# Kernel tuning notes

Measured on AMD Instinct MI355X. Metric: run time of the kernel, lower is better.

The kernel has to match this reference:

```python
import jax, jax.numpy as jnp
import numpy as np

N_RES = 500000


def _rot(vals):
    # stack 9 scalars-per-element into (..., 3, 3) row-major rotation matrices
    return jnp.stack(vals, axis=-1).reshape(*vals[0].shape, 3, 3)


def _dihedral(p0, p1, p2, p3):
    b0 = -(p1 - p0)
    b1 = p2 - p1
    b2 = p3 - p2
    b0xb1 = jnp.cross(b0, b1)
    b1xb2 = jnp.cross(b2, b1)
    y = jnp.sum(jnp.cross(b0xb1, b1xb2) * b1, axis=-1) / jnp.linalg.norm(b1, axis=-1)
    x = jnp.sum(b0xb1 * b1xb2, axis=-1)
    return jnp.nan_to_num(jnp.arctan2(y, x))


def _bb_dihedrals(N, CA, C):
    phi_ = _dihedral(C[:-1], N[1:], CA[1:], C[1:])
    psi_ = _dihedral(N[:-1], CA[:-1], C[:-1], N[1:])
    omg_ = _dihedral(CA[:-1], C[:-1], N[1:], CA[1:])
    pad = jnp.zeros_like(phi_[:1])
    omega = jnp.concatenate([omg_, pad])
    phi = jnp.concatenate([pad, phi_])
    psi = jnp.concatenate([psi_, pad])
    return jnp.stack([omega, phi, psi], axis=-1)  # (n, 3)


def _frames_from_reference(n_xyz, ca_xyz, c_xyz, eps=1e-20):
    # OpenFold Rigid.make_transform_from_reference
    n = n_xyz - ca_xyz
    c = c_xyz - ca_xyz
    cx, cy, cz = c[..., 0], c[..., 1], c[..., 2]
    z = jnp.zeros_like(cx)
    o = jnp.ones_like(cx)
    nrm = jnp.sqrt(eps + cx**2 + cy**2)
    s1, c1 = -cy / nrm, cx / nrm
    R1 = _rot([c1, -s1, z, s1, c1, z, z, z, o])
    nrm2 = jnp.sqrt(eps + cx**2 + cy**2 + cz**2)
    s2, c2 = cz / nrm2, jnp.sqrt(cx**2 + cy**2) / nrm2
    R2 = _rot([c2, z, s2, z, o, z, -s2, z, c2])
    Rc = R2 @ R1
    n2 = jnp.einsum('...ij,...j->...i', Rc, n)
    ny, nz_ = n2[..., 1], n2[..., 2]
    nrm3 = jnp.sqrt(eps + ny**2 + nz_**2)
    sn, cn = -nz_ / nrm3, ny / nrm3
    Rn = _rot([o, z, z, z, cn, -sn, z, sn, cn])
    rots = jnp.swapaxes(Rn @ Rc, -1, -2)
    return rots, ca_xyz  # (n,3,3), (n,3)


def _compose(ra, ta, rb, tb):
    # rigid composition: (ra,ta) o (rb,tb)
    return ra @ rb, jnp.einsum('...ij,...j->...i', ra, tb) + ta


def _forward(aa, bb_coords, sc_torsions, default_frames, group_idx, atom_mask, lit_positions):
    n_xyz, ca_xyz, c_xyz = bb_coords[:, 0], bb_coords[:, 1], bb_coords[:, 2]
    bb_r, bb_t = _frames_from_reference(n_xyz, ca_xyz, c_xyz)

    angles = jnp.concatenate([_bb_dihedrals(n_xyz, ca_xyz, c_xyz), sc_torsions], axis=-1)  # (n,7)
    alpha = jnp.stack([jnp.sin(angles), jnp.cos(angles)], axis=-1)  # (n,7,2) [sin, cos]
    bb_pad = jnp.concatenate([
        jnp.zeros((alpha.shape[0], 1, 1), alpha.dtype),
        jnp.ones((alpha.shape[0], 1, 1), alpha.dtype)], axis=-1)
    alpha = jnp.concatenate([bb_pad, alpha], axis=-2)  # (n,8,2)

    # torsion_angles_to_frames
    d4 = default_frames[aa]            # (n,8,4,4)
    dr, dt = d4[..., :3, :3], d4[..., :3, 3]
    s, cA = alpha[..., 0], alpha[..., 1]
    z = jnp.zeros_like(s)
    o = jnp.ones_like(s)
    Ra = _rot([o, z, z, z, cA, -s, z, s, cA])  # (n,8,3,3) x-axis rotation
    fr = dr @ Ra
    ft = dt
    # chain chi2->chi1, chi3->chi2, chi4->chi3
    r2, t2 = _compose(fr[:, 4], ft[:, 4], fr[:, 5], ft[:, 5])
    r3, t3 = _compose(r2, t2, fr[:, 6], ft[:, 6])
    r4, t4 = _compose(r3, t3, fr[:, 7], ft[:, 7])
    all_r = jnp.concatenate([fr[:, :5], r2[:, None], r3[:, None], r4[:, None]], axis=1)
    all_t = jnp.concatenate([ft[:, :5], t2[:, None], t3[:, None], t4[:, None]], axis=1)
    gr, gt = _compose(bb_r[:, None], bb_t[:, None], all_r, all_t)  # (n,8,3,3), (n,8,3)

    # frames_and_literature_positions_to_atom14_pos (one-hot sum == gather)
    n = aa.shape[0]
    g = group_idx[aa]                   # (n,14)
    ridx = jnp.arange(n)[:, None]
    ar = gr[ridx, g]                    # (n,14,3,3)
    at = gt[ridx, g]                    # (n,14,3)
    lit = lit_positions[aa]             # (n,14,3)
    pred = jnp.einsum('naij,naj->nai', ar, lit) + at
    pred = pred * atom_mask[aa][..., None]

    # use_native_bb_coords=True: keep input backbone atoms
    return jnp.concatenate([bb_coords, pred[:, 4:]], axis=1)  # (n,14,3)


def setup_inputs() -> dict:
    key = jax.random.key(0)
    ks = jax.random.split(key, 7)
    n = N_RES
    aa = jax.random.randint(ks[0], (n,), 0, 21, dtype=jnp.int32)
    bb_coords = jax.random.normal(ks[1], (n, 4, 3), jnp.float32) * 3.0
    sc_torsions = jax.random.uniform(ks[2], (n, 4), jnp.float32, -np.pi, np.pi)
    default_frames = jax.random.normal(ks[3], (21, 8, 4, 4), jnp.float32)
    group_idx = jax.random.randint(ks[4], (21, 14), 0, 8, dtype=jnp.int32)
    atom_mask = (jax.random.uniform(ks[5], (21, 14)) > 0.2).astype(jnp.float32)
    lit_positions = jax.random.normal(ks[6], (21, 14, 3), jnp.float32)
    return {"aa": aa, "bb_coords": bb_coords, "sc_torsions": sc_torsions,
            "default_frames": default_frames, "group_idx": group_idx,
            "atom_mask": atom_mask, "lit_positions": lit_positions}


def reference(aa, bb_coords, sc_torsions, default_frames, group_idx, atom_mask, lit_positions):
    return _forward(aa, bb_coords, sc_torsions, default_frames, group_idx, atom_mask, lit_positions)
```

## Files before the change

kernel.cpp:

```cpp
#include <hip/hip_runtime.h>


struct F3 { float x, y, z; };

__device__ __forceinline__ F3 f3sub(F3 a, F3 b) { return {a.x-b.x, a.y-b.y, a.z-b.z}; }
__device__ __forceinline__ F3 f3cross(F3 a, F3 b) {
    return {a.y*b.z - a.z*b.y, a.z*b.x - a.x*b.z, a.x*b.y - a.y*b.x};
}
__device__ __forceinline__ float f3dot(F3 a, F3 b) { return a.x*b.x + a.y*b.y + a.z*b.z; }

__device__ __forceinline__ void dihedral_sc(F3 p0, F3 p1, F3 p2, F3 p3,
                                            float& s, float& c) {
    F3 b0 = f3sub(p0, p1);
    F3 b1 = f3sub(p2, p1);
    F3 b2 = f3sub(p3, p2);
    F3 u = f3cross(b0, b1);
    F3 v = f3cross(b2, b1);
    F3 w = f3cross(u, v);
    float y = f3dot(w, b1) * rsqrtf(fmaxf(f3dot(b1, b1), 1e-30f));
    float x = f3dot(u, v);
    float r2 = x*x + y*y;
    if (r2 > 1e-24f) {
        float rinv = rsqrtf(r2);
        s = y * rinv;
        c = x * rinv;
    } else {
        s = 0.0f;
        c = 1.0f;
    }
}

#define DF_STRIDE 132
#define LIT_STRIDE 36

__global__ __launch_bounds__(256) void idealizer_kernel(
    const int*   __restrict__ aa,
    const float* __restrict__ bb,
    const float* __restrict__ tor,
    const float* __restrict__ dframes,
    const int*   __restrict__ gidx,
    const float* __restrict__ amask,
    const float* __restrict__ lit,
    float*       __restrict__ out,
    int n)
{
    __shared__ __align__(16) float s_df[21 * DF_STRIDE];
    __shared__ __align__(16) float s_lit[21 * LIT_STRIDE];
    __shared__ __align__(16) float s_out[256 * 42];
    __shared__ unsigned s_gpk[21];
    __shared__ unsigned s_mbit[21];

    const int tid = threadIdx.x;
    for (int j = tid; j < 21 * 128; j += 256)
        s_df[(j >> 7) * DF_STRIDE + (j & 127)] = dframes[j];
    for (int j = tid; j < 21 * 30; j += 256) {
        int a = j / 30, r = j - a * 30;
        s_lit[a * LIT_STRIDE + r] = lit[a * 42 + 12 + r];
    }
    if (tid < 21) {
        unsigned gp = 0, mb = 0;
        #pragma unroll
        for (int a = 0; a < 10; a++) {
            gp |= ((unsigned)gidx[tid * 14 + 4 + a]) << (3 * a);
            mb |= (amask[tid * 14 + 4 + a] != 0.0f ? 1u : 0u) << a;
        }
        s_gpk[tid] = gp;
        s_mbit[tid] = mb;
    }
    __syncthreads();

    for (int i0 = blockIdx.x * 256; i0 < n; i0 += gridDim.x * 256) {
        const int i = i0 + tid;
        if (i < n) {
            float* srow = &s_out[tid * 42];

            const float4* bb4 = (const float4*)bb;
            float4 q0 = bb4[i * 3 + 0];
            float4 q1 = bb4[i * 3 + 1];
            float4 q2 = bb4[i * 3 + 2];
            F3 Np  = {q0.x, q0.y, q0.z};
            F3 CAp = {q0.w, q1.x, q1.y};
            F3 Cp  = {q1.z, q1.w, q2.x};

            float2* s2 = (float2*)srow;
            s2[0] = make_float2(q0.x, q0.y);
            s2[1] = make_float2(q0.z, q0.w);
            s2[2] = make_float2(q1.x, q1.y);
            s2[3] = make_float2(q1.z, q1.w);
            s2[4] = make_float2(q2.x, q2.y);
            s2[5] = make_float2(q2.z, q2.w);

            const int im = (i > 0)     ? i - 1 : 0;
            const int ip = (i < n - 1) ? i + 1 : 0;
            F3 Cm = { bb[im * 12 + 6], bb[im * 12 + 7], bb[im * 12 + 8] };
            float4 r0 = bb4[ip * 3 + 0];
            float2 r1 = ((const float2*)bb)[ip * 6 + 2];
            F3 Nn  = {r0.x, r0.y, r0.z};
            F3 CAn = {r0.w, r1.x, r1.y};

            float s_ph, c_ph, s_ps, c_ps, s_om, c_om;
            dihedral_sc(Cm,  Np,  CAp, Cp,  s_ph, c_ph);
            dihedral_sc(Np,  CAp, Cp,  Nn,  s_ps, c_ps);
            dihedral_sc(CAp, Cp,  Nn,  CAn, s_om, c_om);
            if (i == 0)     { s_ph = 0.0f; c_ph = 1.0f; }
            if (i == n - 1) { s_ps = 0.0f; c_ps = 1.0f; s_om = 0.0f; c_om = 1.0f; }

            const float eps = 1e-20f;
            F3 nv = f3sub(Np, CAp);
            F3 cv = f3sub(Cp, CAp);
            float cx = cv.x, cy = cv.y, cz = cv.z;
            float d2xy  = cx * cx + cy * cy;
            float inrm  = rsqrtf(eps + d2xy);
            float s1 = -cy * inrm, c1 = cx * inrm;
            float inrm2 = rsqrtf(eps + d2xy + cz * cz);
            float s2v = cz * inrm2, c2v = sqrtf(d2xy) * inrm2;
            float Rc00 = c2v * c1,  Rc01 = -c2v * s1, Rc02 = s2v;
            float Rc10 = s1,        Rc11 = c1,        Rc12 = 0.0f;
            float Rc20 = -s2v * c1, Rc21 = s2v * s1,  Rc22 = c2v;
            float n2y = Rc10 * nv.x + Rc11 * nv.y + Rc12 * nv.z;
            float n2z = Rc20 * nv.x + Rc21 * nv.y + Rc22 * nv.z;
            float inrm3 = rsqrtf(eps + n2y * n2y + n2z * n2z);
            float sn = -n2z * inrm3, cn = n2y * inrm3;
            float M10 = cn * Rc10 - sn * Rc20, M11 = cn * Rc11 - sn * Rc21, M12 = cn * Rc12 - sn * Rc22;
            float M20 = sn * Rc10 + cn * Rc20, M21 = sn * Rc11 + cn * Rc21, M22 = sn * Rc12 + cn * Rc22;
            float B00 = Rc00, B01 = M10, B02 = M20;
            float B10 = Rc01, B11 = M11, B12 = M21;
            float B20 = Rc02, B21 = M12, B22 = M22;

            float4 tv = ((const float4*)tor)[i];
            float sang[8], cang[8];
            sang[0] = 0.0f; cang[0] = 1.0f;
            sang[1] = s_om; cang[1] = c_om;
            sang[2] = s_ph; cang[2] = c_ph;
            sang[3] = s_ps; cang[3] = c_ps;
            __sincosf(tv.x, &sang[4], &cang[4]);
            __sincosf(tv.y, &sang[5], &cang[5]);
            __sincosf(tv.z, &sang[6], &cang[6]);
            __sincosf(tv.w, &sang[7], &cang[7]);

            const int aai = aa[i];
            const unsigned gpk  = s_gpk[aai];
            const unsigned mbit = s_mbit[aai];
            const float* lrow = &s_lit[aai * LIT_STRIDE];

            float G00, G01, G02, G10, G11, G12, G20, G21, G22, Gx, Gy, Gz;
            const int dbase = aai * DF_STRIDE;
            #pragma unroll
            for (int g = 0; g < 8; g++) {
                const float4* dfr = (const float4*)&s_df[dbase + g * 16];
                float4 d0 = dfr[0], d1 = dfr[1], d2 = dfr[2];
                float sA = sang[g], cA = cang[g];
                float f00 = d0.x, f01 = cA * d0.y + sA * d0.z, f02 = cA * d0.z - sA * d0.y;
                float f10 = d1.x, f11 = cA * d1.y + sA * d1.z, f12 = cA * d1.z - sA * d1.y;
                float f20 = d2.x, f21 = cA * d2.y + sA * d2.z, f22 = cA * d2.z - sA * d2.y;
                float A00, A01, A02, A10, A11, A12, A20, A21, A22, Atx, Aty, Atz;
                if (g <= 4) {
                    A00 = B00; A01 = B01; A02 = B02;
                    A10 = B10; A11 = B11; A12 = B12;
                    A20 = B20; A21 = B21; A22 = B22;
                    Atx = CAp.x; Aty = CAp.y; Atz = CAp.z;
                } else {
                    A00 = G00; A01 = G01; A02 = G02;
                    A10 = G10; A11 = G11; A12 = G12;
                    A20 = G20; A21 = G21; A22 = G22;
                    Atx = Gx; Aty = Gy; Atz = Gz;
                }
                float n00 = A00 * f00 + A01 * f10 + A02 * f20;
                float n01 = A00 * f01 + A01 * f11 + A02 * f21;
                float n02 = A00 * f02 + A01 * f12 + A02 * f22;
                float n10 = A10 * f00 + A11 * f10 + A12 * f20;
                float n11 = A10 * f01 + A11 * f11 + A12 * f21;
                float n12 = A10 * f02 + A11 * f12 + A12 * f22;
                float n20 = A20 * f00 + A21 * f10 + A22 * f20;
                float n21 = A20 * f01 + A21 * f11 + A22 * f21;
                float n22 = A20 * f02 + A21 * f12 + A22 * f22;
                float ntx = A00 * d0.w + A01 * d1.w + A02 * d2.w + Atx;
                float nty = A10 * d0.w + A11 * d1.w + A12 * d2.w + Aty;
                float ntz = A20 * d0.w + A21 * d1.w + A22 * d2.w + Atz;
                G00 = n00; G01 = n01; G02 = n02;
                G10 = n10; G11 = n11; G12 = n12;
                G20 = n20; G21 = n21; G22 = n22;
                Gx = ntx; Gy = nty; Gz = ntz;

                #pragma unroll
                for (int a = 0; a < 10; a++) {
                    bool sel = ((gpk >> (3 * a)) & 7u) == (unsigned)g;
                    if (sel) {
                        float mk = ((mbit >> a) & 1u) ? 1.0f : 0.0f;
                        float lx = lrow[3*a], ly = lrow[3*a+1], lz = lrow[3*a+2];
                        float px = fmaf(G00, lx, fmaf(G01, ly, fmaf(G02, lz, Gx)));
                        float py = fmaf(G10, lx, fmaf(G11, ly, fmaf(G12, lz, Gy)));
                        float pz = fmaf(G20, lx, fmaf(G21, ly, fmaf(G22, lz, Gz)));
                        float* po = srow + 12 + 3 * a;
                        po[0] = mk * px;
                        po[1] = mk * py;
                        po[2] = mk * pz;
                    }
                }
            }
        }

        __syncthreads();

        int m = n - i0; if (m > 256) m = 256;
        const int cnt2 = m * 21;
        float2* gout = (float2*)(out + (size_t)i0 * 42);
        const float2* l2 = (const float2*)s_out;
        for (int off = tid; off < cnt2; off += 256)
            gout[off] = l2[off];

        __syncthreads();
    }
}

extern "C" void kernel_launch(void* const* d_in, const int* in_sizes, int n_in,
                              void* d_out, int out_size, void* d_ws, size_t ws_size,
                              hipStream_t stream) {
    const int*   aa  = (const int*)d_in[0];
    const float* bb  = (const float*)d_in[1];
    const float* tor = (const float*)d_in[2];
    const float* df  = (const float*)d_in[3];
    const int*   gi  = (const int*)d_in[4];
    const float* am  = (const float*)d_in[5];
    const float* lp  = (const float*)d_in[6];
    float* outp = (float*)d_out;
    const int n = in_sizes[0];
    int tiles = (n + 255) / 256;
    int blocks = tiles < 1024 ? tiles : 1024;
    idealizer_kernel<<<blocks, 256, 0, stream>>>(aa, bb, tor, df, gi, am, lp, outp, n);
}
```

Measured before the change: 156.0 us.

## Store default frames in fp16 LDS, shrink output tile, reorder frame composition

Default frames are converted to half precision in shared memory, the per-thread output staging shrinks to the 30 sidechain floats, and backbone coordinates are copied straight from global memory during the coalesced store. The composition chain now builds local frames and applies the backbone rotation once per atom, which adds a 3x3 transform per atom. Launch bounds request four blocks per CU. The aim is to cut LDS use and registers so more blocks fit per CU, at the cost of fp16 rounding error in the frame constants and extra FMAs.

```diff
diff --git a/kernel.cpp b/kernel.cpp
--- a/kernel.cpp
+++ b/kernel.cpp
@@ -1,4 +1,5 @@
 #include <hip/hip_runtime.h>
+#include <hip/hip_fp16.h>
 
 
 struct F3 { float x, y, z; };
@@ -30,10 +31,10 @@
     }
 }
 
-#define DF_STRIDE 132
-#define LIT_STRIDE 36
-
-__global__ __launch_bounds__(256) void idealizer_kernel(
+#define LIT_STRIDE 30
+#define OT_STRIDE  30
+
+__global__ __launch_bounds__(256, 4) void idealizer_kernel(
     const int*   __restrict__ aa,
     const float* __restrict__ bb,
     const float* __restrict__ tor,
@@ -44,15 +45,17 @@
     float*       __restrict__ out,
     int n)
 {
-    __shared__ __align__(16) float s_df[21 * DF_STRIDE];
-    __shared__ __align__(16) float s_lit[21 * LIT_STRIDE];
-    __shared__ __align__(16) float s_out[256 * 42];
+    __shared__ __align__(16) float  s_ot[256 * OT_STRIDE];
+    __shared__ __align__(8)  __half s_dfh[21 * 8 * 12];
+    __shared__ __align__(16) float  s_lit[21 * LIT_STRIDE];
     __shared__ unsigned s_gpk[21];
     __shared__ unsigned s_mbit[21];
 
     const int tid = threadIdx.x;
-    for (int j = tid; j < 21 * 128; j += 256)
-        s_df[(j >> 7) * DF_STRIDE + (j & 127)] = dframes[j];
+    for (int j = tid; j < 21 * 8 * 12; j += 256) {
+        int blk = j / 12, e = j - blk * 12;
+        s_dfh[j] = __float2half(dframes[blk * 16 + e]);
+    }
     for (int j = tid; j < 21 * 30; j += 256) {
         int a = j / 30, r = j - a * 30;
         s_lit[a * LIT_STRIDE + r] = lit[a * 42 + 12 + r];
@@ -72,23 +75,13 @@
     for (int i0 = blockIdx.x * 256; i0 < n; i0 += gridDim.x * 256) {
         const int i = i0 + tid;
         if (i < n) {
-            float* srow = &s_out[tid * 42];
-
             const float4* bb4 = (const float4*)bb;
             float4 q0 = bb4[i * 3 + 0];
             float4 q1 = bb4[i * 3 + 1];
-            float4 q2 = bb4[i * 3 + 2];
+            float Cz  = bb[i * 12 + 8];
             F3 Np  = {q0.x, q0.y, q0.z};
             F3 CAp = {q0.w, q1.x, q1.y};
-            F3 Cp  = {q1.z, q1.w, q2.x};
-
-            float2* s2 = (float2*)srow;
-            s2[0] = make_float2(q0.x, q0.y);
-            s2[1] = make_float2(q0.z, q0.w);
-            s2[2] = make_float2(q1.x, q1.y);
-            s2[3] = make_float2(q1.z, q1.w);
-            s2[4] = make_float2(q2.x, q2.y);
-            s2[5] = make_float2(q2.z, q2.w);
+            F3 Cp  = {q1.z, q1.w, Cz};
 
             const int im = (i > 0)     ? i - 1 : 0;
             const int ip = (i < n - 1) ? i + 1 : 0;
@@ -142,45 +135,46 @@
             const unsigned gpk  = s_gpk[aai];
             const unsigned mbit = s_mbit[aai];
             const float* lrow = &s_lit[aai * LIT_STRIDE];
-
-            float G00, G01, G02, G10, G11, G12, G20, G21, G22, Gx, Gy, Gz;
-            const int dbase = aai * DF_STRIDE;
+            float* srow = &s_ot[tid * OT_STRIDE];
+
+            float L00, L01, L02, L10, L11, L12, L20, L21, L22, Lx, Ly, Lz;
+            const __half2* dfa = (const __half2*)(s_dfh + (size_t)aai * 96);
             #pragma unroll
             for (int g = 0; g < 8; g++) {
-                const float4* dfr = (const float4*)&s_df[dbase + g * 16];
-                float4 d0 = dfr[0], d1 = dfr[1], d2 = dfr[2];
+                const __half2* dh = dfa + g * 6;
+                float2 e0 = __half22float2(dh[0]), e1 = __half22float2(dh[1]);
+                float2 e2 = __half22float2(dh[2]), e3 = __half22float2(dh[3]);
+                float2 e4 = __half22float2(dh[4]), e5 = __half22float2(dh[5]);
+                float m00 = e0.x, m01 = e0.y, m02 = e1.x, tx = e1.y;
+                float m10 = e2.x, m11 = e2.y, m12 = e3.x, ty = e3.y;
+                float m20 = e4.x, m21 = e4.y, m22 = e5.x, tz = e5.y;
                 float sA = sang[g], cA = cang[g];
-                float f00 = d0.x, f01 = cA * d0.y + sA * d0.z, f02 = cA * d0.z - sA * d0.y;
-                float f10 = d1.x, f11 = cA * d1.y + sA * d1.z, f12 = cA * d1.z - sA * d1.y;
-                float f20 = d2.x, f21 = cA * d2.y + sA * d2.z, f22 = cA * d2.z - sA * d2.y;
-                float A00, A01, A02, A10, A11, A12, A20, A21, A22, Atx, Aty, Atz;
+                float f00 = m00, f01 = cA * m01 + sA * m02, f02 = cA * m02 - sA * m01;
+                float f10 = m10, f11 = cA * m11 + sA * m12, f12 = cA * m12 - sA * m11;
+                float f20 = m20, f21 = cA * m21 + sA * m22, f22 = cA * m22 - sA * m21;
                 if (g <= 4) {
-                    A00 = B00; A01 = B01; A02 = B02;
-                    A10 = B10; A11 = B11; A12 = B12;
-                    A20 = B20; A21 = B21; A22 = B22;
-                    Atx = CAp.x; Aty = CAp.y; Atz = CAp.z;
+                    L00 = f00; L01 = f01; L02 = f02;
+                    L10 = f10; L11 = f11; L12 = f12;
+                    L20 = f20; L21 = f21; L22 = f22;
+                    Lx = tx; Ly = ty; Lz = tz;
                 } else {
-                    A00 = G00; A01 = G01; A02 = G02;
-                    A10 = G10; A11 = G11; A12 = G12;
-                    A20 = G20; A21 = G21; A22 = G22;
-                    Atx = Gx; Aty = Gy; Atz = Gz;
+                    float n00 = L00 * f00 + L01 * f10 + L02 * f20;
+                    float n01 = L00 * f01 + L01 * f11 + L02 * f21;
+                    float n02 = L00 * f02 + L01 * f12 + L02 * f22;
+                    float n10 = L10 * f00 + L11 * f10 + L12 * f20;
+                    float n11 = L10 * f01 + L11 * f11 + L12 * f21;
+                    float n12 = L10 * f02 + L11 * f12 + L12 * f22;
+                    float n20 = L20 * f00 + L21 * f10 + L22 * f20;
+                    float n21 = L20 * f01 + L21 * f11 + L22 * f21;
+                    float n22 = L20 * f02 + L21 * f12 + L22 * f22;
+                    float ntx = L00 * tx + L01 * ty + L02 * tz + Lx;
+                    float nty = L10 * tx + L11 * ty + L12 * tz + Ly;
+                    float ntz = L20 * tx + L21 * ty + L22 * tz + Lz;
+                    L00 = n00; L01 = n01; L02 = n02;
+                    L10 = n10; L11 = n11; L12 = n12;
+                    L20 = n20; L21 = n21; L22 = n22;
+                    Lx = ntx; Ly = nty; Lz = ntz;
                 }
-                float n00 = A00 * f00 + A01 * f10 + A02 * f20;
-                float n01 = A00 * f01 + A01 * f11 + A02 * f21;
-                float n02 = A00 * f02 + A01 * f12 + A02 * f22;
-                float n10 = A10 * f00 + A11 * f10 + A12 * f20;
-                float n11 = A10 * f01 + A11 * f11 + A12 * f21;
-                float n12 = A10 * f02 + A11 * f12 + A12 * f22;
-                float n20 = A20 * f00 + A21 * f10 + A22 * f20;
-                float n21 = A20 * f01 + A21 * f11 + A22 * f21;
-                float n22 = A20 * f02 + A21 * f12 + A22 * f22;
-                float ntx = A00 * d0.w + A01 * d1.w + A02 * d2.w + Atx;
-                float nty = A10 * d0.w + A11 * d1.w + A12 * d2.w + Aty;
-                float ntz = A20 * d0.w + A21 * d1.w + A22 * d2.w + Atz;
-                G00 = n00; G01 = n01; G02 = n02;
-                G10 = n10; G11 = n11; G12 = n12;
-                G20 = n20; G21 = n21; G22 = n22;
-                Gx = ntx; Gy = nty; Gz = ntz;
 
                 #pragma unroll
                 for (int a = 0; a < 10; a++) {
@@ -188,10 +182,13 @@
                     if (sel) {
                         float mk = ((mbit >> a) & 1u) ? 1.0f : 0.0f;
                         float lx = lrow[3*a], ly = lrow[3*a+1], lz = lrow[3*a+2];
-                        float px = fmaf(G00, lx, fmaf(G01, ly, fmaf(G02, lz, Gx)));
-                        float py = fmaf(G10, lx, fmaf(G11, ly, fmaf(G12, lz, Gy)));
-                        float pz = fmaf(G20, lx, fmaf(G21, ly, fmaf(G22, lz, Gz)));
-                        float* po = srow + 12 + 3 * a;
+                        float qx = fmaf(L00, lx, fmaf(L01, ly, fmaf(L02, lz, Lx)));
+                        float qy = fmaf(L10, lx, fmaf(L11, ly, fmaf(L12, lz, Ly)));
+                        float qz = fmaf(L20, lx, fmaf(L21, ly, fmaf(L22, lz, Lz)));
+                        float px = fmaf(B00, qx, fmaf(B01, qy, fmaf(B02, qz, CAp.x)));
+                        float py = fmaf(B10, qx, fmaf(B11, qy, fmaf(B12, qz, CAp.y)));
+                        float pz = fmaf(B20, qx, fmaf(B21, qy, fmaf(B22, qz, CAp.z)));
+                        float* po = srow + 3 * a;
                         po[0] = mk * px;
                         po[1] = mk * py;
                         po[2] = mk * pz;
@@ -205,9 +202,18 @@
         int m = n - i0; if (m > 256) m = 256;
         const int cnt2 = m * 21;
         float2* gout = (float2*)(out + (size_t)i0 * 42);
-        const float2* l2 = (const float2*)s_out;
-        for (int off = tid; off < cnt2; off += 256)
-            gout[off] = l2[off];
+        const float2* bbt = (const float2*)(bb + (size_t)i0 * 12);
+        for (int off = tid; off < cnt2; off += 256) {
+            int r = off / 21, j = off - r * 21;
+            float2 val;
+            if (j < 6) {
+                val = bbt[r * 6 + j];
+            } else {
+                const float* tp = &s_ot[r * OT_STRIDE + 2 * (j - 6)];
+                val = make_float2(tp[0], tp[1]);
+            }
+            gout[off] = val;
+        }
 
         __syncthreads();
     }
```

After: 156.6 us. Within noise of the previous version (+0.4%).
